# Optimization experiments

Hardware: AMD Instinct MI355X
Metric: run time of the kernel (lower is better)

Reference implementation:

```python
import jax, jax.numpy as jnp
import numpy as np

N_NODES = 50000
N_EDGES = 600000
N_FEAT = 64
D = 128
N_GRAPHS = 1024
N_LAYERS = 4


def setup_inputs() -> dict:
    key = jax.random.key(0)
    ks = jax.random.split(key, 16)
    x = jax.random.normal(ks[0], (N_NODES, N_FEAT), dtype=jnp.float32)
    edge_index = jax.random.randint(ks[1], (2, N_EDGES), 0, N_NODES, dtype=jnp.int64)
    batch_index = jnp.sort(jax.random.randint(ks[2], (N_NODES,), 0, N_GRAPHS, dtype=jnp.int64))
    def lin(k, fan_in, fan_out):
        s = 1.0 / np.sqrt(fan_in)
        kw, kb = jax.random.split(k)
        w = jax.random.uniform(kw, (fan_in, fan_out), minval=-s, maxval=s, dtype=jnp.float32)
        b = jax.random.uniform(kb, (fan_out,), minval=-s, maxval=s, dtype=jnp.float32)
        return w, b
    w0, b0 = lin(ks[3], N_FEAT, D)
    w1, b1 = lin(ks[4], D, D)
    w2, b2 = lin(ks[5], D, D)
    w3, b3 = lin(ks[6], D, D)
    wp, bp = lin(ks[7], D, D)
    return {"x": x, "edge_index": edge_index, "batch_index": batch_index,
            "w0": w0, "b0": b0, "w1": w1, "b1": b1, "w2": w2, "b2": b2,
            "w3": w3, "b3": b3, "wp": wp, "bp": bp}


def _gin_layer(x, src, dst, w, b):
    # GINConv with eps=0: MLP(x_i + sum_{j in N(i)} x_j); MLP = Linear -> ReLU
    agg = jax.ops.segment_sum(x[src], dst, num_segments=N_NODES)
    return jax.nn.relu((x + agg) @ w + b)


def reference(x, edge_index, batch_index, w0, b0, w1, b1, w2, b2, w3, b3, wp, bp):
    src, dst = edge_index[0], edge_index[1]
    # first layer changes width 64 -> 128; agg happens in input width
    agg0 = jax.ops.segment_sum(x[src], dst, num_segments=N_NODES)
    h = jax.nn.relu((x + agg0) @ w0 + b0)
    for w, b in ((w1, b1), (w2, b2), (w3, b3)):
        h = _gin_layer(h, src, dst, w, b)
    # global mean pool per graph
    sums = jax.ops.segment_sum(h, batch_index, num_segments=N_GRAPHS)
    counts = jax.ops.segment_sum(jnp.ones((N_NODES,), dtype=h.dtype), batch_index, num_segments=N_GRAPHS)
    pooled = sums / jnp.maximum(counts, 1.0)[:, None]
    # post_mp: Linear -> ReLU (dropout identity at inference)
    return jax.nn.relu(pooled @ wp + bp)
```

## Files before the change

### kernel.cpp

```cpp
#include <hip/hip_runtime.h>
#include <hip/hip_fp16.h>


#define N_NODES  50000
#define N_EDGES  600000
#define N_FEAT   64
#define DIM      128
#define N_GRAPHS 1024
#define NC       7
#define CSH      13
#define TOT2     (N_NODES * NC)
#define SCH      2048
#define NBLK     ((TOT2 + SCH - 1) / SCH)
#define TPB      256
#define GT128    ((N_NODES + 127) / 128)

typedef _Float16 f16x8 __attribute__((ext_vector_type(8)));
typedef float    f32x4 __attribute__((ext_vector_type(4)));

#define CNTZ2 (TOT2 / 4)
#define XWORK (N_NODES * N_FEAT / 4)
#define PREP_TOTAL (CNTZ2 + XWORK + N_FEAT * DIM + 3 * DIM * DIM)

__global__ __launch_bounds__(TPB) void prep_k(
    const float* __restrict__ x, __half* __restrict__ xh,
    const float* __restrict__ w0, const float* __restrict__ w1,
    const float* __restrict__ w2, const float* __restrict__ w3,
    __half* __restrict__ Wt0, __half* __restrict__ Wt1,
    __half* __restrict__ Wt2, __half* __restrict__ Wt3,
    int* __restrict__ cnt2) {
  int i = blockIdx.x * TPB + threadIdx.x;
  if (i < CNTZ2) {
    *reinterpret_cast<int4*>(cnt2 + i * 4) = make_int4(0, 0, 0, 0);
    return;
  }
  i -= CNTZ2;
  if (i < XWORK) {
    float4 v = *reinterpret_cast<const float4*>(x + (size_t)i * 4);
    union { __half2 h2[2]; uint2 u; } pk;
    pk.h2[0] = __floats2half2_rn(v.x, v.y);
    pk.h2[1] = __floats2half2_rn(v.z, v.w);
    *reinterpret_cast<uint2*>(xh + (size_t)i * 4) = pk.u;
    return;
  }
  int j = i - XWORK;
  if (j < N_FEAT * DIM) {
    int k = j >> 7, n = j & 127;
    Wt0[n * N_FEAT + k] = __float2half(w0[j]);
    return;
  }
  j -= N_FEAT * DIM;
  if (j >= 3 * DIM * DIM) return;
  int wsel = j / (DIM * DIM);
  int jj = j - wsel * (DIM * DIM);
  int k = jj >> 7, n = jj & 127;
  const float* W = (wsel == 0) ? w1 : (wsel == 1) ? w2 : w3;
  __half* Wt     = (wsel == 0) ? Wt1 : (wsel == 1) ? Wt2 : Wt3;
  Wt[n * DIM + k] = __float2half(W[jj]);
}

__global__ __launch_bounds__(TPB) void hist_k(
    const int* __restrict__ src, const int* __restrict__ dst,
    int* __restrict__ cnt2) {
  int e = blockIdx.x * TPB + threadIdx.x;
  if (e >= N_EDGES) return;
  int key = dst[e] * NC + (src[e] >> CSH);
  atomicAdd(&cnt2[key], 1);
}

__global__ __launch_bounds__(TPB) void scan_part_k(
    const int* __restrict__ cnt2, int* __restrict__ part) {
  __shared__ int ws[4];
  int t = threadIdx.x, b = blockIdx.x;
  int base = b * SCH + t * 8;
  int s = 0;
  if (base < TOT2) {
    int4 a = *reinterpret_cast<const int4*>(cnt2 + base);
    int4 c = *reinterpret_cast<const int4*>(cnt2 + base + 4);
    s = a.x + a.y + a.z + a.w + c.x + c.y + c.z + c.w;
  }
  for (int off = 32; off; off >>= 1) s += __shfl_down(s, off, 64);
  int lane = t & 63, wv = t >> 6;
  if (lane == 0) ws[wv] = s;
  __syncthreads();
  if (t == 0) part[b] = ws[0] + ws[1] + ws[2] + ws[3];
}

__global__ __launch_bounds__(TPB) void scan_write_k(
    const int* __restrict__ cnt2, const int* __restrict__ part,
    int* __restrict__ row_ptr2, int* __restrict__ fill2) {
  __shared__ int pscan[TPB];
  __shared__ int wsum[4];
  int t = threadIdx.x, b = blockIdx.x;
  int lane = t & 63, wv = t >> 6;
  int base = b * SCH + t * 8;

  if (base < TOT2) {
    *reinterpret_cast<int4*>(fill2 + base) = make_int4(0, 0, 0, 0);
    *reinterpret_cast<int4*>(fill2 + base + 4) = make_int4(0, 0, 0, 0);
  }

  pscan[t] = (t < NBLK) ? part[t] : 0;
  __syncthreads();
  for (int off = 1; off < TPB; off <<= 1) {
    int v = (t >= off) ? pscan[t - off] : 0;
    __syncthreads();
    pscan[t] += v;
    __syncthreads();
  }
  int blk_off = (b > 0) ? pscan[b - 1] : 0;

  int v[8] = {0,0,0,0,0,0,0,0};
  if (base < TOT2) {
    int4 a = *reinterpret_cast<const int4*>(cnt2 + base);
    int4 c = *reinterpret_cast<const int4*>(cnt2 + base + 4);
    v[0]=a.x; v[1]=a.y; v[2]=a.z; v[3]=a.w;
    v[4]=c.x; v[5]=c.y; v[6]=c.z; v[7]=c.w;
  }
  int ls = 0;
#pragma unroll
  for (int i = 0; i < 8; ++i) ls += v[i];
  int incl = ls;
  for (int off = 1; off < 64; off <<= 1) {
    int u = __shfl_up(incl, off, 64);
    if (lane >= off) incl += u;
  }
  if (lane == 63) wsum[wv] = incl;
  __syncthreads();
  int woff = 0;
  for (int w = 0; w < wv; ++w) woff += wsum[w];
  int run = blk_off + woff + (incl - ls);
  if (base < TOT2) {
    int rp[8];
#pragma unroll
    for (int i = 0; i < 8; ++i) { rp[i] = run; run += v[i]; }
    *reinterpret_cast<int4*>(row_ptr2 + base) = make_int4(rp[0], rp[1], rp[2], rp[3]);
    *reinterpret_cast<int4*>(row_ptr2 + base + 4) = make_int4(rp[4], rp[5], rp[6], rp[7]);
  }
  if (b == 0 && t == 0) row_ptr2[TOT2] = N_EDGES;
}

__global__ __launch_bounds__(TPB) void fill_k(
    const int* __restrict__ src, const int* __restrict__ dst,
    const int* __restrict__ row_ptr2, int* __restrict__ fill2,
    int* __restrict__ csr_src) {
  int e = blockIdx.x * TPB + threadIdx.x;
  if (e >= N_EDGES) return;
  int s = src[e];
  int key = dst[e] * NC + (s >> CSH);
  int pos = row_ptr2[key] + atomicAdd(&fill2[key], 1);
  csr_src[pos] = s;
}

template<int K, bool EPI>
__global__ __launch_bounds__(TPB) void gemm_k(
    const __half* __restrict__ A, const __half* __restrict__ Wt,
    const float* __restrict__ bias, __half* __restrict__ y) {
  constexpr int KP = K + 8;
  constexpr int OSP = 144;
  constexpr int NKC = K / 32;
  constexpr size_t WSZ = (size_t)128 * KP * sizeof(__half);
  constexpr size_t OSZ = (size_t)128 * OSP * sizeof(__half);
  __shared__ __align__(16) char smem[WSZ > OSZ ? WSZ : OSZ];
  __half (*Ws)[KP]  = reinterpret_cast<__half(*)[KP]>(smem);
  __half (*Os)[OSP] = reinterpret_cast<__half(*)[OSP]>(smem);

  int tid = threadIdx.x;
  int w = tid >> 6, lane = tid & 63;
  int quad = lane >> 4, m = lane & 15;
  int row0 = blockIdx.x * 128;

  for (int i = tid; i < 128 * (K / 8); i += TPB) {
    int r = i / (K / 8), c = (i % (K / 8)) * 8;
    *reinterpret_cast<f16x8*>(&Ws[r][c]) =
        *reinterpret_cast<const f16x8*>(Wt + (size_t)r * K + c);
  }

  f16x8 areg[2][NKC];
#pragma unroll
  for (int s = 0; s < 2; ++s) {
    int row = row0 + w * 32 + s * 16 + m;
    row = min(row, N_NODES - 1);
    const f16x8* Ar = reinterpret_cast<const f16x8*>(A + (size_t)row * K);
#pragma unroll
    for (int kc = 0; kc < NKC; ++kc)
      areg[s][kc] = Ar[kc * 4 + quad];
  }
  __syncthreads();

  f32x4 acc[2][8];
#pragma unroll
  for (int s = 0; s < 2; ++s)
#pragma unroll
    for (int t = 0; t < 8; ++t) acc[s][t] = (f32x4){0.f, 0.f, 0.f, 0.f};

#pragma unroll
  for (int kc = 0; kc < NKC; ++kc) {
#pragma unroll
    for (int t = 0; t < 8; ++t) {
      f16x8 b = *reinterpret_cast<const f16x8*>(&Ws[t * 16 + m][kc * 32 + quad * 8]);
      acc[0][t] = __builtin_amdgcn_mfma_f32_16x16x32_f16(areg[0][kc], b, acc[0][t], 0, 0, 0);
      acc[1][t] = __builtin_amdgcn_mfma_f32_16x16x32_f16(areg[1][kc], b, acc[1][t], 0, 0, 0);
    }
  }

  __syncthreads();

#pragma unroll
  for (int t = 0; t < 8; ++t) {
    float bv = EPI ? bias[t * 16 + m] : 0.f;
#pragma unroll
    for (int s = 0; s < 2; ++s)
#pragma unroll
      for (int r = 0; r < 4; ++r) {
        float v = acc[s][t][r];
        if (EPI) v = fmaxf(v + bv, 0.f);
        Os[w * 32 + s * 16 + quad * 4 + r][t * 16 + m] = __float2half(v);
      }
  }
  __syncthreads();

#pragma unroll
  for (int it = 0; it < 8; ++it) {
    int i = tid + it * TPB;
    int r = i >> 4, c = (i & 15) * 8;
    int row = row0 + r;
    if (row < N_NODES)
      *reinterpret_cast<f16x8*>(y + (size_t)row * 128 + c) =
          *reinterpret_cast<const f16x8*>(&Os[r][c]);
  }
}

template<int F, bool BR>
__global__ __launch_bounds__(TPB) void gather_k(
    const __half* __restrict__ y, const int* __restrict__ row_ptr2,
    const int* __restrict__ csr_src, const float* __restrict__ bias,
    __half* __restrict__ hout) {
  constexpr int CH = F / 8;
  const f16x8* yv = reinterpret_cast<const f16x8*>(y);
  int gid  = blockIdx.x * TPB + threadIdx.x;
  int node = gid / CH;
  int l    = gid % CH;
  if (node >= N_NODES) return;
  int beg = row_ptr2[node * NC];
  int end = row_ptr2[node * NC + NC];

  f16x8 self = yv[(size_t)node * CH + l];
  float acc[8];
#pragma unroll
  for (int v = 0; v < 8; ++v) acc[v] = (float)self[v];

  int e = beg;
  for (; e + 3 < end; e += 4) {
    int s0 = csr_src[e+0], s1 = csr_src[e+1], s2 = csr_src[e+2], s3 = csr_src[e+3];
    f16x8 v0 = yv[(size_t)s0 * CH + l];
    f16x8 v1 = yv[(size_t)s1 * CH + l];
    f16x8 v2 = yv[(size_t)s2 * CH + l];
    f16x8 v3 = yv[(size_t)s3 * CH + l];
#pragma unroll
    for (int v = 0; v < 8; ++v)
      acc[v] += ((float)v0[v] + (float)v1[v]) + ((float)v2[v] + (float)v3[v]);
  }
  for (; e < end; ++e) {
    f16x8 v0 = yv[(size_t)csr_src[e] * CH + l];
#pragma unroll
    for (int v = 0; v < 8; ++v) acc[v] += (float)v0[v];
  }

  f16x8 o;
  if (BR) {
    float4 b0 = *reinterpret_cast<const float4*>(bias + l * 8);
    float4 b1 = *reinterpret_cast<const float4*>(bias + l * 8 + 4);
    float bb[8] = {b0.x, b0.y, b0.z, b0.w, b1.x, b1.y, b1.z, b1.w};
#pragma unroll
    for (int v = 0; v < 8; ++v) o[v] = (_Float16)fmaxf(acc[v] + bb[v], 0.f);
  } else {
#pragma unroll
    for (int v = 0; v < 8; ++v) o[v] = (_Float16)acc[v];
  }
  reinterpret_cast<f16x8*>(hout)[(size_t)node * CH + l] = o;
}

__global__ __launch_bounds__(128) void pool_post_k(
    const __half* __restrict__ h, const int* __restrict__ batch,
    const float* __restrict__ W, const float* __restrict__ bias,
    float* __restrict__ out) {
  __shared__ float xs[DIM];
  int g = blockIdx.x;
  int col = threadIdx.x;
  int lo = 0, hi = N_NODES;
  while (lo < hi) { int mid = (lo + hi) >> 1; if (batch[mid] < g) lo = mid + 1; else hi = mid; }
  int beg = lo;
  hi = N_NODES;
  while (lo < hi) { int mid = (lo + hi) >> 1; if (batch[mid] < g + 1) lo = mid + 1; else hi = mid; }
  int end = lo;

  float acc = 0.f;
  for (int n = beg; n < end; ++n) acc += __half2float(h[(size_t)n * DIM + col]);
  float cnt = fmaxf((float)(end - beg), 1.0f);
  xs[col] = acc / cnt;
  __syncthreads();
  float o = bias[col];
  for (int k = 0; k < DIM; ++k)
    o = fmaf(xs[k], W[(size_t)k * DIM + col], o);
  out[(size_t)g * DIM + col] = fmaxf(o, 0.f);
}

extern "C" void kernel_launch(void* const* d_in, const int* in_sizes, int n_in,
                              void* d_out, int out_size, void* d_ws, size_t ws_size,
                              hipStream_t stream) {
  const float* x    = (const float*)d_in[0];
  const int*   ei   = (const int*)d_in[1];
  const int*   batch= (const int*)d_in[2];
  const float* w0 = (const float*)d_in[3];  const float* b0 = (const float*)d_in[4];
  const float* w1 = (const float*)d_in[5];  const float* b1 = (const float*)d_in[6];
  const float* w2 = (const float*)d_in[7];  const float* b2 = (const float*)d_in[8];
  const float* w3 = (const float*)d_in[9];  const float* b3 = (const float*)d_in[10];
  const float* wp = (const float*)d_in[11]; const float* bp = (const float*)d_in[12];
  float* out = (float*)d_out;

  const int* src = ei;
  const int* dst = ei + N_EDGES;

  __half* xh = (__half*)d_ws;
  __half* y  = xh + (size_t)N_NODES * N_FEAT;
  __half* h  = y  + (size_t)N_NODES * DIM;
  __half* Wt0 = h + (size_t)N_NODES * DIM;
  __half* Wt1 = Wt0 + N_FEAT * DIM;
  __half* Wt2 = Wt1 + DIM * DIM;
  __half* Wt3 = Wt2 + DIM * DIM;
  int* cnt2     = (int*)(Wt3 + DIM * DIM);
  int* fill2    = cnt2 + TOT2;
  int* part     = fill2 + TOT2;
  int* row_ptr2 = part + 256;
  int* csr_src  = row_ptr2 + (TOT2 + 1);
  __half* s = y;

  prep_k<<<(PREP_TOTAL + TPB - 1) / TPB, TPB, 0, stream>>>(
      x, xh, w0, w1, w2, w3, Wt0, Wt1, Wt2, Wt3, cnt2);
  hist_k<<<(N_EDGES + TPB - 1) / TPB, TPB, 0, stream>>>(src, dst, cnt2);
  scan_part_k <<<NBLK, TPB, 0, stream>>>(cnt2, part);
  scan_write_k<<<NBLK, TPB, 0, stream>>>(cnt2, part, row_ptr2, fill2);
  fill_k<<<(N_EDGES + TPB - 1) / TPB, TPB, 0, stream>>>(src, dst, row_ptr2,
                                                        fill2, csr_src);

  gather_k<N_FEAT, false><<<(N_NODES * 8 + TPB - 1) / TPB, TPB, 0, stream>>>(
      xh, row_ptr2, csr_src, nullptr, s);
  gemm_k<N_FEAT, true><<<GT128, TPB, 0, stream>>>(s, Wt0, b0, h);

  const __half* Wl[3] = {Wt1, Wt2, Wt3};
  const float*  Bl[3] = {b1, b2, b3};
  for (int l = 0; l < 3; ++l) {
    gemm_k<DIM, false><<<GT128, TPB, 0, stream>>>(h, Wl[l], nullptr, y);
    gather_k<DIM, true><<<(N_NODES * 16 + TPB - 1) / TPB, TPB, 0, stream>>>(
        y, row_ptr2, csr_src, Bl[l], h);
  }

  pool_post_k<<<N_GRAPHS, 128, 0, stream>>>(h, batch, wp, bp, out);
}
```

Before: 302.3 us.

## Fuse all stages into one persistent cooperative kernel with grid syncs

Replaces the sequence of about a dozen separate kernel launches with a single cooperative persistent kernel. Phases are separated by grid-wide barriers and each phase uses grid-stride loops. The scan's second pass now computes block offsets by summing partials directly instead of a shared-memory scan, and pooling handles two graphs per block. This removes launch overhead and inter-kernel gaps. In exchange it adds grid.sync costs, caps occupancy because the fused kernel carries the largest register and shared-memory footprint of any phase, and reloads the GEMM weights for every tile.

Measured after the change: 1.136 ms. 3.76x slower.

```diff
diff --git a/kernel.cpp b/kernel.cpp
--- a/kernel.cpp
+++ b/kernel.cpp
@@ -1,5 +1,8 @@
 #include <hip/hip_runtime.h>
 #include <hip/hip_fp16.h>
+#include <hip/hip_cooperative_groups.h>
+
+namespace cg = cooperative_groups;
 
 
 #define N_NODES  50000
@@ -14,347 +17,365 @@
 #define NBLK     ((TOT2 + SCH - 1) / SCH)
 #define TPB      256
 #define GT128    ((N_NODES + 127) / 128)
+#define NCU      256
 
 typedef _Float16 f16x8 __attribute__((ext_vector_type(8)));
 typedef float    f32x4 __attribute__((ext_vector_type(4)));
 
 #define CNTZ2 (TOT2 / 4)
 #define XWORK (N_NODES * N_FEAT / 4)
-#define PREP_TOTAL (CNTZ2 + XWORK + N_FEAT * DIM + 3 * DIM * DIM)
-
-__global__ __launch_bounds__(TPB) void prep_k(
-    const float* __restrict__ x, __half* __restrict__ xh,
-    const float* __restrict__ w0, const float* __restrict__ w1,
-    const float* __restrict__ w2, const float* __restrict__ w3,
-    __half* __restrict__ Wt0, __half* __restrict__ Wt1,
-    __half* __restrict__ Wt2, __half* __restrict__ Wt3,
-    int* __restrict__ cnt2) {
-  int i = blockIdx.x * TPB + threadIdx.x;
-  if (i < CNTZ2) {
-    *reinterpret_cast<int4*>(cnt2 + i * 4) = make_int4(0, 0, 0, 0);
-    return;
-  }
-  i -= CNTZ2;
-  if (i < XWORK) {
-    float4 v = *reinterpret_cast<const float4*>(x + (size_t)i * 4);
-    union { __half2 h2[2]; uint2 u; } pk;
-    pk.h2[0] = __floats2half2_rn(v.x, v.y);
-    pk.h2[1] = __floats2half2_rn(v.z, v.w);
-    *reinterpret_cast<uint2*>(xh + (size_t)i * 4) = pk.u;
-    return;
-  }
-  int j = i - XWORK;
-  if (j < N_FEAT * DIM) {
-    int k = j >> 7, n = j & 127;
-    Wt0[n * N_FEAT + k] = __float2half(w0[j]);
-    return;
-  }
-  j -= N_FEAT * DIM;
-  if (j >= 3 * DIM * DIM) return;
-  int wsel = j / (DIM * DIM);
-  int jj = j - wsel * (DIM * DIM);
-  int k = jj >> 7, n = jj & 127;
-  const float* W = (wsel == 0) ? w1 : (wsel == 1) ? w2 : w3;
-  __half* Wt     = (wsel == 0) ? Wt1 : (wsel == 1) ? Wt2 : Wt3;
-  Wt[n * DIM + k] = __float2half(W[jj]);
-}
-
-__global__ __launch_bounds__(TPB) void hist_k(
-    const int* __restrict__ src, const int* __restrict__ dst,
-    int* __restrict__ cnt2) {
-  int e = blockIdx.x * TPB + threadIdx.x;
-  if (e >= N_EDGES) return;
-  int key = dst[e] * NC + (src[e] >> CSH);
-  atomicAdd(&cnt2[key], 1);
-}
-
-__global__ __launch_bounds__(TPB) void scan_part_k(
-    const int* __restrict__ cnt2, int* __restrict__ part) {
-  __shared__ int ws[4];
-  int t = threadIdx.x, b = blockIdx.x;
-  int base = b * SCH + t * 8;
-  int s = 0;
-  if (base < TOT2) {
-    int4 a = *reinterpret_cast<const int4*>(cnt2 + base);
-    int4 c = *reinterpret_cast<const int4*>(cnt2 + base + 4);
-    s = a.x + a.y + a.z + a.w + c.x + c.y + c.z + c.w;
-  }
-  for (int off = 32; off; off >>= 1) s += __shfl_down(s, off, 64);
-  int lane = t & 63, wv = t >> 6;
-  if (lane == 0) ws[wv] = s;
-  __syncthreads();
-  if (t == 0) part[b] = ws[0] + ws[1] + ws[2] + ws[3];
-}
-
-__global__ __launch_bounds__(TPB) void scan_write_k(
-    const int* __restrict__ cnt2, const int* __restrict__ part,
-    int* __restrict__ row_ptr2, int* __restrict__ fill2) {
-  __shared__ int pscan[TPB];
-  __shared__ int wsum[4];
-  int t = threadIdx.x, b = blockIdx.x;
-  int lane = t & 63, wv = t >> 6;
-  int base = b * SCH + t * 8;
-
-  if (base < TOT2) {
-    *reinterpret_cast<int4*>(fill2 + base) = make_int4(0, 0, 0, 0);
-    *reinterpret_cast<int4*>(fill2 + base + 4) = make_int4(0, 0, 0, 0);
-  }
-
-  pscan[t] = (t < NBLK) ? part[t] : 0;
-  __syncthreads();
-  for (int off = 1; off < TPB; off <<= 1) {
-    int v = (t >= off) ? pscan[t - off] : 0;
-    __syncthreads();
-    pscan[t] += v;
-    __syncthreads();
-  }
-  int blk_off = (b > 0) ? pscan[b - 1] : 0;
-
-  int v[8] = {0,0,0,0,0,0,0,0};
-  if (base < TOT2) {
-    int4 a = *reinterpret_cast<const int4*>(cnt2 + base);
-    int4 c = *reinterpret_cast<const int4*>(cnt2 + base + 4);
-    v[0]=a.x; v[1]=a.y; v[2]=a.z; v[3]=a.w;
-    v[4]=c.x; v[5]=c.y; v[6]=c.z; v[7]=c.w;
-  }
-  int ls = 0;
-#pragma unroll
-  for (int i = 0; i < 8; ++i) ls += v[i];
-  int incl = ls;
-  for (int off = 1; off < 64; off <<= 1) {
-    int u = __shfl_up(incl, off, 64);
-    if (lane >= off) incl += u;
-  }
-  if (lane == 63) wsum[wv] = incl;
-  __syncthreads();
-  int woff = 0;
-  for (int w = 0; w < wv; ++w) woff += wsum[w];
-  int run = blk_off + woff + (incl - ls);
-  if (base < TOT2) {
-    int rp[8];
-#pragma unroll
-    for (int i = 0; i < 8; ++i) { rp[i] = run; run += v[i]; }
-    *reinterpret_cast<int4*>(row_ptr2 + base) = make_int4(rp[0], rp[1], rp[2], rp[3]);
-    *reinterpret_cast<int4*>(row_ptr2 + base + 4) = make_int4(rp[4], rp[5], rp[6], rp[7]);
-  }
-  if (b == 0 && t == 0) row_ptr2[TOT2] = N_EDGES;
-}
-
-__global__ __launch_bounds__(TPB) void fill_k(
-    const int* __restrict__ src, const int* __restrict__ dst,
-    const int* __restrict__ row_ptr2, int* __restrict__ fill2,
-    int* __restrict__ csr_src) {
-  int e = blockIdx.x * TPB + threadIdx.x;
-  if (e >= N_EDGES) return;
-  int s = src[e];
-  int key = dst[e] * NC + (s >> CSH);
-  int pos = row_ptr2[key] + atomicAdd(&fill2[key], 1);
-  csr_src[pos] = s;
+#define PREP_TOTAL (2 * CNTZ2 + XWORK + N_FEAT * DIM + 3 * DIM * DIM)
+
+#define SMEM_BYTES 36864
+
+struct MegaArgs {
+  const float* x; const int* src; const int* dst; const int* batch;
+  const float *w0, *b0, *w1, *b1, *w2, *b2, *w3, *b3, *wp, *bp;
+  float* out;
+  __half *xh, *y, *h, *Wt0, *Wt1, *Wt2, *Wt3;
+  int *cnt2, *fill2, *part, *row_ptr2, *csr_src;
+};
+
+__device__ void scan_part_phase(const int* __restrict__ cnt2,
+                                int* __restrict__ part, char* smem) {
+  int* ws = reinterpret_cast<int*>(smem);
+  int t = threadIdx.x, lane = t & 63, wv = t >> 6;
+  for (int pb = blockIdx.x; pb < NBLK; pb += gridDim.x) {
+    int base = pb * SCH + t * 8;
+    int s = 0;
+    if (base < TOT2) {
+      int4 aa = *reinterpret_cast<const int4*>(cnt2 + base);
+      int4 cc = *reinterpret_cast<const int4*>(cnt2 + base + 4);
+      s = aa.x + aa.y + aa.z + aa.w + cc.x + cc.y + cc.z + cc.w;
+    }
+    for (int off = 32; off; off >>= 1) s += __shfl_down(s, off, 64);
+    if (lane == 0) ws[wv] = s;
+    __syncthreads();
+    if (t == 0) part[pb] = ws[0] + ws[1] + ws[2] + ws[3];
+    __syncthreads();
+  }
+}
+
+__device__ void scan_write_phase(const int* __restrict__ cnt2,
+                                 const int* __restrict__ part,
+                                 int* __restrict__ row_ptr2, char* smem) {
+  int* sh = reinterpret_cast<int*>(smem);
+  int t = threadIdx.x, lane = t & 63, wv = t >> 6;
+  for (int pb = blockIdx.x; pb < NBLK; pb += gridDim.x) {
+    int v = (t < pb) ? part[t] : 0;
+    for (int off = 32; off; off >>= 1) v += __shfl_down(v, off, 64);
+    if (lane == 0) sh[wv] = v;
+    __syncthreads();
+    int blk_off = sh[0] + sh[1] + sh[2] + sh[3];
+    __syncthreads();
+
+    int base = pb * SCH + t * 8;
+    int vals[8] = {0,0,0,0,0,0,0,0};
+    if (base < TOT2) {
+      int4 aa = *reinterpret_cast<const int4*>(cnt2 + base);
+      int4 cc = *reinterpret_cast<const int4*>(cnt2 + base + 4);
+      vals[0]=aa.x; vals[1]=aa.y; vals[2]=aa.z; vals[3]=aa.w;
+      vals[4]=cc.x; vals[5]=cc.y; vals[6]=cc.z; vals[7]=cc.w;
+    }
+    int ls = 0;
+#pragma unroll
+    for (int i2 = 0; i2 < 8; ++i2) ls += vals[i2];
+    int incl = ls;
+    for (int off = 1; off < 64; off <<= 1) {
+      int u = __shfl_up(incl, off, 64);
+      if (lane >= off) incl += u;
+    }
+    if (lane == 63) sh[4 + wv] = incl;
+    __syncthreads();
+    int woff = 0;
+    for (int w2 = 0; w2 < wv; ++w2) woff += sh[4 + w2];
+    int run = blk_off + woff + (incl - ls);
+    if (base < TOT2) {
+      int rp[8];
+#pragma unroll
+      for (int i2 = 0; i2 < 8; ++i2) { rp[i2] = run; run += vals[i2]; }
+      *reinterpret_cast<int4*>(row_ptr2 + base) = make_int4(rp[0],rp[1],rp[2],rp[3]);
+      *reinterpret_cast<int4*>(row_ptr2 + base + 4) = make_int4(rp[4],rp[5],rp[6],rp[7]);
+    }
+    __syncthreads();
+  }
+  if (blockIdx.x == 0 && threadIdx.x == 0) row_ptr2[TOT2] = N_EDGES;
 }
 
 template<int K, bool EPI>
-__global__ __launch_bounds__(TPB) void gemm_k(
-    const __half* __restrict__ A, const __half* __restrict__ Wt,
-    const float* __restrict__ bias, __half* __restrict__ y) {
+__device__ void gemm_phase(const __half* __restrict__ A,
+                           const __half* __restrict__ Wt,
+                           const float* __restrict__ bias,
+                           __half* __restrict__ yOut, char* smem) {
   constexpr int KP = K + 8;
   constexpr int OSP = 144;
   constexpr int NKC = K / 32;
-  constexpr size_t WSZ = (size_t)128 * KP * sizeof(__half);
-  constexpr size_t OSZ = (size_t)128 * OSP * sizeof(__half);
-  __shared__ __align__(16) char smem[WSZ > OSZ ? WSZ : OSZ];
   __half (*Ws)[KP]  = reinterpret_cast<__half(*)[KP]>(smem);
   __half (*Os)[OSP] = reinterpret_cast<__half(*)[OSP]>(smem);
-
   int tid = threadIdx.x;
   int w = tid >> 6, lane = tid & 63;
   int quad = lane >> 4, m = lane & 15;
-  int row0 = blockIdx.x * 128;
-
-  for (int i = tid; i < 128 * (K / 8); i += TPB) {
-    int r = i / (K / 8), c = (i % (K / 8)) * 8;
-    *reinterpret_cast<f16x8*>(&Ws[r][c]) =
-        *reinterpret_cast<const f16x8*>(Wt + (size_t)r * K + c);
-  }
-
-  f16x8 areg[2][NKC];
-#pragma unroll
-  for (int s = 0; s < 2; ++s) {
-    int row = row0 + w * 32 + s * 16 + m;
-    row = min(row, N_NODES - 1);
-    const f16x8* Ar = reinterpret_cast<const f16x8*>(A + (size_t)row * K);
-#pragma unroll
-    for (int kc = 0; kc < NKC; ++kc)
-      areg[s][kc] = Ar[kc * 4 + quad];
-  }
-  __syncthreads();
-
-  f32x4 acc[2][8];
-#pragma unroll
-  for (int s = 0; s < 2; ++s)
-#pragma unroll
-    for (int t = 0; t < 8; ++t) acc[s][t] = (f32x4){0.f, 0.f, 0.f, 0.f};
-
-#pragma unroll
-  for (int kc = 0; kc < NKC; ++kc) {
+  for (int tile = blockIdx.x; tile < GT128; tile += gridDim.x) {
+    int row0 = tile * 128;
+    for (int i = tid; i < 128 * (K / 8); i += TPB) {
+      int r = i / (K / 8), c = (i % (K / 8)) * 8;
+      *reinterpret_cast<f16x8*>(&Ws[r][c]) =
+          *reinterpret_cast<const f16x8*>(Wt + (size_t)r * K + c);
+    }
+    f16x8 areg[2][NKC];
+#pragma unroll
+    for (int s = 0; s < 2; ++s) {
+      int row = row0 + w * 32 + s * 16 + m;
+      row = min(row, N_NODES - 1);
+      const f16x8* Ar = reinterpret_cast<const f16x8*>(A + (size_t)row * K);
+#pragma unroll
+      for (int kc = 0; kc < NKC; ++kc) areg[s][kc] = Ar[kc * 4 + quad];
+    }
+    __syncthreads();
+
+    f32x4 acc[2][8];
+#pragma unroll
+    for (int s = 0; s < 2; ++s)
+#pragma unroll
+      for (int t = 0; t < 8; ++t) acc[s][t] = (f32x4){0.f, 0.f, 0.f, 0.f};
+
+#pragma unroll
+    for (int kc = 0; kc < NKC; ++kc) {
+#pragma unroll
+      for (int t = 0; t < 8; ++t) {
+        f16x8 b = *reinterpret_cast<const f16x8*>(&Ws[t * 16 + m][kc * 32 + quad * 8]);
+        acc[0][t] = __builtin_amdgcn_mfma_f32_16x16x32_f16(areg[0][kc], b, acc[0][t], 0, 0, 0);
+        acc[1][t] = __builtin_amdgcn_mfma_f32_16x16x32_f16(areg[1][kc], b, acc[1][t], 0, 0, 0);
+      }
+    }
+    __syncthreads();
+
 #pragma unroll
     for (int t = 0; t < 8; ++t) {
-      f16x8 b = *reinterpret_cast<const f16x8*>(&Ws[t * 16 + m][kc * 32 + quad * 8]);
-      acc[0][t] = __builtin_amdgcn_mfma_f32_16x16x32_f16(areg[0][kc], b, acc[0][t], 0, 0, 0);
-      acc[1][t] = __builtin_amdgcn_mfma_f32_16x16x32_f16(areg[1][kc], b, acc[1][t], 0, 0, 0);
-    }
-  }
-
-  __syncthreads();
-
-#pragma unroll
-  for (int t = 0; t < 8; ++t) {
-    float bv = EPI ? bias[t * 16 + m] : 0.f;
-#pragma unroll
-    for (int s = 0; s < 2; ++s)
-#pragma unroll
-      for (int r = 0; r < 4; ++r) {
-        float v = acc[s][t][r];
-        if (EPI) v = fmaxf(v + bv, 0.f);
-        Os[w * 32 + s * 16 + quad * 4 + r][t * 16 + m] = __float2half(v);
-      }
-  }
-  __syncthreads();
-
-#pragma unroll
-  for (int it = 0; it < 8; ++it) {
-    int i = tid + it * TPB;
-    int r = i >> 4, c = (i & 15) * 8;
-    int row = row0 + r;
-    if (row < N_NODES)
-      *reinterpret_cast<f16x8*>(y + (size_t)row * 128 + c) =
-          *reinterpret_cast<const f16x8*>(&Os[r][c]);
+      float bv = EPI ? bias[t * 16 + m] : 0.f;
+#pragma unroll
+      for (int s = 0; s < 2; ++s)
+#pragma unroll
+        for (int r = 0; r < 4; ++r) {
+          float v = acc[s][t][r];
+          if (EPI) v = fmaxf(v + bv, 0.f);
+          Os[w * 32 + s * 16 + quad * 4 + r][t * 16 + m] = __float2half(v);
+        }
+    }
+    __syncthreads();
+
+#pragma unroll
+    for (int it = 0; it < 8; ++it) {
+      int i = tid + it * TPB;
+      int r = i >> 4, c = (i & 15) * 8;
+      int row = row0 + r;
+      if (row < N_NODES)
+        *reinterpret_cast<f16x8*>(yOut + (size_t)row * 128 + c) =
+            *reinterpret_cast<const f16x8*>(&Os[r][c]);
+    }
+    __syncthreads();
   }
 }
 
 template<int F, bool BR>
-__global__ __launch_bounds__(TPB) void gather_k(
-    const __half* __restrict__ y, const int* __restrict__ row_ptr2,
-    const int* __restrict__ csr_src, const float* __restrict__ bias,
-    __half* __restrict__ hout) {
+__device__ void gather_phase(const __half* __restrict__ yin,
+                             const int* __restrict__ row_ptr2,
+                             const int* __restrict__ csr_src,
+                             const float* __restrict__ bias,
+                             __half* __restrict__ hout) {
   constexpr int CH = F / 8;
-  const f16x8* yv = reinterpret_cast<const f16x8*>(y);
-  int gid  = blockIdx.x * TPB + threadIdx.x;
-  int node = gid / CH;
-  int l    = gid % CH;
-  if (node >= N_NODES) return;
-  int beg = row_ptr2[node * NC];
-  int end = row_ptr2[node * NC + NC];
-
-  f16x8 self = yv[(size_t)node * CH + l];
-  float acc[8];
-#pragma unroll
-  for (int v = 0; v < 8; ++v) acc[v] = (float)self[v];
-
-  int e = beg;
-  for (; e + 3 < end; e += 4) {
-    int s0 = csr_src[e+0], s1 = csr_src[e+1], s2 = csr_src[e+2], s3 = csr_src[e+3];
-    f16x8 v0 = yv[(size_t)s0 * CH + l];
-    f16x8 v1 = yv[(size_t)s1 * CH + l];
-    f16x8 v2 = yv[(size_t)s2 * CH + l];
-    f16x8 v3 = yv[(size_t)s3 * CH + l];
-#pragma unroll
-    for (int v = 0; v < 8; ++v)
-      acc[v] += ((float)v0[v] + (float)v1[v]) + ((float)v2[v] + (float)v3[v]);
-  }
-  for (; e < end; ++e) {
-    f16x8 v0 = yv[(size_t)csr_src[e] * CH + l];
-#pragma unroll
-    for (int v = 0; v < 8; ++v) acc[v] += (float)v0[v];
-  }
-
-  f16x8 o;
-  if (BR) {
-    float4 b0 = *reinterpret_cast<const float4*>(bias + l * 8);
-    float4 b1 = *reinterpret_cast<const float4*>(bias + l * 8 + 4);
-    float bb[8] = {b0.x, b0.y, b0.z, b0.w, b1.x, b1.y, b1.z, b1.w};
-#pragma unroll
-    for (int v = 0; v < 8; ++v) o[v] = (_Float16)fmaxf(acc[v] + bb[v], 0.f);
-  } else {
-#pragma unroll
-    for (int v = 0; v < 8; ++v) o[v] = (_Float16)acc[v];
-  }
-  reinterpret_cast<f16x8*>(hout)[(size_t)node * CH + l] = o;
-}
-
-__global__ __launch_bounds__(128) void pool_post_k(
-    const __half* __restrict__ h, const int* __restrict__ batch,
-    const float* __restrict__ W, const float* __restrict__ bias,
-    float* __restrict__ out) {
-  __shared__ float xs[DIM];
-  int g = blockIdx.x;
-  int col = threadIdx.x;
-  int lo = 0, hi = N_NODES;
-  while (lo < hi) { int mid = (lo + hi) >> 1; if (batch[mid] < g) lo = mid + 1; else hi = mid; }
-  int beg = lo;
-  hi = N_NODES;
-  while (lo < hi) { int mid = (lo + hi) >> 1; if (batch[mid] < g + 1) lo = mid + 1; else hi = mid; }
-  int end = lo;
-
-  float acc = 0.f;
-  for (int n = beg; n < end; ++n) acc += __half2float(h[(size_t)n * DIM + col]);
-  float cnt = fmaxf((float)(end - beg), 1.0f);
-  xs[col] = acc / cnt;
-  __syncthreads();
-  float o = bias[col];
-  for (int k = 0; k < DIM; ++k)
-    o = fmaf(xs[k], W[(size_t)k * DIM + col], o);
-  out[(size_t)g * DIM + col] = fmaxf(o, 0.f);
+  const f16x8* yv = reinterpret_cast<const f16x8*>(yin);
+  const int total = N_NODES * CH;
+  for (int gid = blockIdx.x * TPB + threadIdx.x; gid < total;
+       gid += gridDim.x * TPB) {
+    int node = gid / CH;
+    int l    = gid % CH;
+    int beg = row_ptr2[node * NC];
+    int end = row_ptr2[node * NC + NC];
+
+    f16x8 self = yv[(size_t)node * CH + l];
+    float acc[8];
+#pragma unroll
+    for (int v = 0; v < 8; ++v) acc[v] = (float)self[v];
+
+    int e = beg;
+    for (; e + 3 < end; e += 4) {
+      int s0 = csr_src[e+0], s1 = csr_src[e+1], s2 = csr_src[e+2], s3 = csr_src[e+3];
+      f16x8 v0 = yv[(size_t)s0 * CH + l];
+      f16x8 v1 = yv[(size_t)s1 * CH + l];
+      f16x8 v2 = yv[(size_t)s2 * CH + l];
+      f16x8 v3 = yv[(size_t)s3 * CH + l];
+#pragma unroll
+      for (int v = 0; v < 8; ++v)
+        acc[v] += ((float)v0[v] + (float)v1[v]) + ((float)v2[v] + (float)v3[v]);
+    }
+    for (; e < end; ++e) {
+      f16x8 v0 = yv[(size_t)csr_src[e] * CH + l];
+#pragma unroll
+      for (int v = 0; v < 8; ++v) acc[v] += (float)v0[v];
+    }
+
+    f16x8 o;
+    if (BR) {
+      float4 b0 = *reinterpret_cast<const float4*>(bias + l * 8);
+      float4 b1 = *reinterpret_cast<const float4*>(bias + l * 8 + 4);
+      float bb[8] = {b0.x, b0.y, b0.z, b0.w, b1.x, b1.y, b1.z, b1.w};
+#pragma unroll
+      for (int v = 0; v < 8; ++v) o[v] = (_Float16)fmaxf(acc[v] + bb[v], 0.f);
+    } else {
+#pragma unroll
+      for (int v = 0; v < 8; ++v) o[v] = (_Float16)acc[v];
+    }
+    reinterpret_cast<f16x8*>(hout)[(size_t)node * CH + l] = o;
+  }
+}
+
+__device__ void pool_phase(const __half* __restrict__ h, const int* __restrict__ batch,
+                           const float* __restrict__ W, const float* __restrict__ bias,
+                           float* __restrict__ out, char* smem) {
+  float* xs = reinterpret_cast<float*>(smem);
+  int t = threadIdx.x;
+  int sub = t >> 7, col = t & 127;
+  for (int gp = blockIdx.x; gp < N_GRAPHS / 2; gp += gridDim.x) {
+    int g = gp * 2 + sub;
+    int lo = 0, hi = N_NODES;
+    while (lo < hi) { int mid = (lo + hi) >> 1; if (batch[mid] < g) lo = mid + 1; else hi = mid; }
+    int beg = lo;
+    hi = N_NODES;
+    while (lo < hi) { int mid = (lo + hi) >> 1; if (batch[mid] < g + 1) lo = mid + 1; else hi = mid; }
+    int end = lo;
+    float acc = 0.f;
+    for (int n = beg; n < end; ++n) acc += __half2float(h[(size_t)n * DIM + col]);
+    float cnt = fmaxf((float)(end - beg), 1.0f);
+    xs[sub * DIM + col] = acc / cnt;
+    __syncthreads();
+    float o = bias[col];
+    for (int k = 0; k < DIM; ++k)
+      o = fmaf(xs[sub * DIM + k], W[(size_t)k * DIM + col], o);
+    out[(size_t)g * DIM + col] = fmaxf(o, 0.f);
+    __syncthreads();
+  }
+}
+
+__global__ __launch_bounds__(TPB, 4) void mega_k(MegaArgs a) {
+  __shared__ __align__(16) char smem[SMEM_BYTES];
+  cg::grid_group grid = cg::this_grid();
+  const int gstride = gridDim.x * TPB;
+  const int gtid = blockIdx.x * TPB + threadIdx.x;
+
+  for (int i = gtid; i < PREP_TOTAL; i += gstride) {
+    int j = i;
+    if (j < CNTZ2) {
+      *reinterpret_cast<int4*>(a.cnt2 + j * 4) = make_int4(0, 0, 0, 0);
+      continue;
+    }
+    j -= CNTZ2;
+    if (j < CNTZ2) {
+      *reinterpret_cast<int4*>(a.fill2 + j * 4) = make_int4(0, 0, 0, 0);
+      continue;
+    }
+    j -= CNTZ2;
+    if (j < XWORK) {
+      float4 v = *reinterpret_cast<const float4*>(a.x + (size_t)j * 4);
+      union { __half2 h2[2]; uint2 u; } pk;
+      pk.h2[0] = __floats2half2_rn(v.x, v.y);
+      pk.h2[1] = __floats2half2_rn(v.z, v.w);
+      *reinterpret_cast<uint2*>(a.xh + (size_t)j * 4) = pk.u;
+      continue;
+    }
+    j -= XWORK;
+    if (j < N_FEAT * DIM) {
+      int k = j >> 7, n = j & 127;
+      a.Wt0[n * N_FEAT + k] = __float2half(a.w0[j]);
+      continue;
+    }
+    j -= N_FEAT * DIM;
+    int wsel = j / (DIM * DIM);
+    int jj = j - wsel * (DIM * DIM);
+    int k = jj >> 7, n = jj & 127;
+    const float* W = (wsel == 0) ? a.w1 : (wsel == 1) ? a.w2 : a.w3;
+    __half* Wt     = (wsel == 0) ? a.Wt1 : (wsel == 1) ? a.Wt2 : a.Wt3;
+    Wt[n * DIM + k] = __float2half(W[jj]);
+  }
+  grid.sync();
+
+  for (int e = gtid; e < N_EDGES; e += gstride)
+    atomicAdd(&a.cnt2[a.dst[e] * NC + (a.src[e] >> CSH)], 1);
+  grid.sync();
+
+  scan_part_phase(a.cnt2, a.part, smem);
+  grid.sync();
+  scan_write_phase(a.cnt2, a.part, a.row_ptr2, smem);
+  grid.sync();
+
+  for (int e = gtid; e < N_EDGES; e += gstride) {
+    int s = a.src[e];
+    int key = a.dst[e] * NC + (s >> CSH);
+    int pos = a.row_ptr2[key] + atomicAdd(&a.fill2[key], 1);
+    a.csr_src[pos] = s;
+  }
+  grid.sync();
+
+  gather_phase<N_FEAT, false>(a.xh, a.row_ptr2, a.csr_src, nullptr, a.y);
+  grid.sync();
+  gemm_phase<N_FEAT, true>(a.y, a.Wt0, a.b0, a.h, smem);
+  grid.sync();
+
+#pragma unroll 1
+  for (int l = 0; l < 3; ++l) {
+    const __half* Wt = (l == 0) ? a.Wt1 : (l == 1) ? a.Wt2 : a.Wt3;
+    const float*  bb = (l == 0) ? a.b1  : (l == 1) ? a.b2  : a.b3;
+    gemm_phase<DIM, false>(a.h, Wt, nullptr, a.y, smem);
+    grid.sync();
+    gather_phase<DIM, true>(a.y, a.row_ptr2, a.csr_src, bb, a.h);
+    grid.sync();
+  }
+
+  pool_phase(a.h, a.batch, a.wp, a.bp, a.out, smem);
 }
 
 extern "C" void kernel_launch(void* const* d_in, const int* in_sizes, int n_in,
                               void* d_out, int out_size, void* d_ws, size_t ws_size,
                               hipStream_t stream) {
-  const float* x    = (const float*)d_in[0];
-  const int*   ei   = (const int*)d_in[1];
-  const int*   batch= (const int*)d_in[2];
-  const float* w0 = (const float*)d_in[3];  const float* b0 = (const float*)d_in[4];
-  const float* w1 = (const float*)d_in[5];  const float* b1 = (const float*)d_in[6];
-  const float* w2 = (const float*)d_in[7];  const float* b2 = (const float*)d_in[8];
-  const float* w3 = (const float*)d_in[9];  const float* b3 = (const float*)d_in[10];
-  const float* wp = (const float*)d_in[11]; const float* bp = (const float*)d_in[12];
-  float* out = (float*)d_out;
-
-  const int* src = ei;
-  const int* dst = ei + N_EDGES;
-
-  __half* xh = (__half*)d_ws;
-  __half* y  = xh + (size_t)N_NODES * N_FEAT;
-  __half* h  = y  + (size_t)N_NODES * DIM;
-  __half* Wt0 = h + (size_t)N_NODES * DIM;
-  __half* Wt1 = Wt0 + N_FEAT * DIM;
-  __half* Wt2 = Wt1 + DIM * DIM;
-  __half* Wt3 = Wt2 + DIM * DIM;
-  int* cnt2     = (int*)(Wt3 + DIM * DIM);
-  int* fill2    = cnt2 + TOT2;
-  int* part     = fill2 + TOT2;
-  int* row_ptr2 = part + 256;
-  int* csr_src  = row_ptr2 + (TOT2 + 1);
-  __half* s = y;
-
-  prep_k<<<(PREP_TOTAL + TPB - 1) / TPB, TPB, 0, stream>>>(
-      x, xh, w0, w1, w2, w3, Wt0, Wt1, Wt2, Wt3, cnt2);
-  hist_k<<<(N_EDGES + TPB - 1) / TPB, TPB, 0, stream>>>(src, dst, cnt2);
-  scan_part_k <<<NBLK, TPB, 0, stream>>>(cnt2, part);
-  scan_write_k<<<NBLK, TPB, 0, stream>>>(cnt2, part, row_ptr2, fill2);
-  fill_k<<<(N_EDGES + TPB - 1) / TPB, TPB, 0, stream>>>(src, dst, row_ptr2,
-                                                        fill2, csr_src);
-
-  gather_k<N_FEAT, false><<<(N_NODES * 8 + TPB - 1) / TPB, TPB, 0, stream>>>(
-      xh, row_ptr2, csr_src, nullptr, s);
-  gemm_k<N_FEAT, true><<<GT128, TPB, 0, stream>>>(s, Wt0, b0, h);
-
-  const __half* Wl[3] = {Wt1, Wt2, Wt3};
-  const float*  Bl[3] = {b1, b2, b3};
-  for (int l = 0; l < 3; ++l) {
-    gemm_k<DIM, false><<<GT128, TPB, 0, stream>>>(h, Wl[l], nullptr, y);
-    gather_k<DIM, true><<<(N_NODES * 16 + TPB - 1) / TPB, TPB, 0, stream>>>(
-        y, row_ptr2, csr_src, Bl[l], h);
-  }
-
-  pool_post_k<<<N_GRAPHS, 128, 0, stream>>>(h, batch, wp, bp, out);
-}
+  MegaArgs a;
+  a.x = (const float*)d_in[0];
+  const int* ei = (const int*)d_in[1];
+  a.src = ei; a.dst = ei + N_EDGES;
+  a.batch = (const int*)d_in[2];
+  a.w0 = (const float*)d_in[3];  a.b0 = (const float*)d_in[4];
+  a.w1 = (const float*)d_in[5];  a.b1 = (const float*)d_in[6];
+  a.w2 = (const float*)d_in[7];  a.b2 = (const float*)d_in[8];
+  a.w3 = (const float*)d_in[9];  a.b3 = (const float*)d_in[10];
+  a.wp = (const float*)d_in[11]; a.bp = (const float*)d_in[12];
+  a.out = (float*)d_out;
+
+  __half* p = (__half*)d_ws;
+  a.xh  = p; p += (size_t)N_NODES * N_FEAT;
+  a.y   = p; p += (size_t)N_NODES * DIM;
+  a.h   = p; p += (size_t)N_NODES * DIM;
+  a.Wt0 = p; p += N_FEAT * DIM;
+  a.Wt1 = p; p += DIM * DIM;
+  a.Wt2 = p; p += DIM * DIM;
+  a.Wt3 = p; p += DIM * DIM;
+  int* q = (int*)p;
+  a.cnt2     = q; q += TOT2;
+  a.fill2    = q; q += TOT2;
+  a.part     = q; q += 256;
+  a.row_ptr2 = q; q += TOT2 + 1;
+  a.csr_src  = q;
+
+  static int s_grid = 0;
+  if (s_grid == 0) {
+    int bpc = 0;
+    if (hipOccupancyMaxActiveBlocksPerMultiprocessor(
+            &bpc, (const void*)mega_k, TPB, 0) != hipSuccess || bpc < 1)
+      bpc = 1;
+    long g = (long)bpc * NCU;
+    if (g > 2048) g = 2048;
+    s_grid = (int)g;
+  }
+
+  void* params[] = { (void*)&a };
+  hipLaunchCooperativeKernel((const void*)mega_k, dim3(s_grid), dim3(TPB),
+                             params, 0, stream);
+}
```

## Drop fill array by atomically bumping row pointers; add compact node row_ptr

Applied to the files above, without the earlier changes.

The CSR build no longer keeps a separate fill-counter array. fill_k now atomically increments row_ptr2 itself to get each edge's slot, which removes zeroing one array and one extra read per edge. scan_write_k also writes a compact per-node row_ptr, so the gather kernels read pointers at stride 1 instead of stride NC. The gather loop gains an 8-way unrolled path to keep more neighbor loads in flight, at the cost of more registers.

After: 305.4 us. About the same (+1.0%).

```diff
diff --git a/kernel.cpp b/kernel.cpp
--- a/kernel.cpp
+++ b/kernel.cpp
@@ -88,17 +88,12 @@
 
 __global__ __launch_bounds__(TPB) void scan_write_k(
     const int* __restrict__ cnt2, const int* __restrict__ part,
-    int* __restrict__ row_ptr2, int* __restrict__ fill2) {
+    int* __restrict__ row_ptr2, int* __restrict__ row_ptr) {
   __shared__ int pscan[TPB];
   __shared__ int wsum[4];
   int t = threadIdx.x, b = blockIdx.x;
   int lane = t & 63, wv = t >> 6;
   int base = b * SCH + t * 8;
-
-  if (base < TOT2) {
-    *reinterpret_cast<int4*>(fill2 + base) = make_int4(0, 0, 0, 0);
-    *reinterpret_cast<int4*>(fill2 + base + 4) = make_int4(0, 0, 0, 0);
-  }
 
   pscan[t] = (t < NBLK) ? part[t] : 0;
   __syncthreads();
@@ -136,19 +131,23 @@
     for (int i = 0; i < 8; ++i) { rp[i] = run; run += v[i]; }
     *reinterpret_cast<int4*>(row_ptr2 + base) = make_int4(rp[0], rp[1], rp[2], rp[3]);
     *reinterpret_cast<int4*>(row_ptr2 + base + 4) = make_int4(rp[4], rp[5], rp[6], rp[7]);
-  }
-  if (b == 0 && t == 0) row_ptr2[TOT2] = N_EDGES;
+#pragma unroll
+    for (int i = 0; i < 8; ++i) {
+      int bin = base + i;
+      if (bin % NC == 0) row_ptr[bin / NC] = rp[i];
+    }
+  }
+  if (b == 0 && t == 0) row_ptr[N_NODES] = N_EDGES;
 }
 
 __global__ __launch_bounds__(TPB) void fill_k(
     const int* __restrict__ src, const int* __restrict__ dst,
-    const int* __restrict__ row_ptr2, int* __restrict__ fill2,
-    int* __restrict__ csr_src) {
+    int* __restrict__ row_ptr2, int* __restrict__ csr_src) {
   int e = blockIdx.x * TPB + threadIdx.x;
   if (e >= N_EDGES) return;
   int s = src[e];
   int key = dst[e] * NC + (s >> CSH);
-  int pos = row_ptr2[key] + atomicAdd(&fill2[key], 1);
+  int pos = atomicAdd(&row_ptr2[key], 1);
   csr_src[pos] = s;
 }
 
@@ -233,7 +232,7 @@
 
 template<int F, bool BR>
 __global__ __launch_bounds__(TPB) void gather_k(
-    const __half* __restrict__ y, const int* __restrict__ row_ptr2,
+    const __half* __restrict__ y, const int* __restrict__ row_ptr,
     const int* __restrict__ csr_src, const float* __restrict__ bias,
     __half* __restrict__ hout) {
   constexpr int CH = F / 8;
@@ -242,8 +241,8 @@
   int node = gid / CH;
   int l    = gid % CH;
   if (node >= N_NODES) return;
-  int beg = row_ptr2[node * NC];
-  int end = row_ptr2[node * NC + NC];
+  int beg = row_ptr[node];
+  int end = row_ptr[node + 1];
 
   f16x8 self = yv[(size_t)node * CH + l];
   float acc[8];
@@ -251,6 +250,22 @@
   for (int v = 0; v < 8; ++v) acc[v] = (float)self[v];
 
   int e = beg;
+  for (; e + 7 < end; e += 8) {
+    int s0 = csr_src[e+0], s1 = csr_src[e+1], s2 = csr_src[e+2], s3 = csr_src[e+3];
+    int s4 = csr_src[e+4], s5 = csr_src[e+5], s6 = csr_src[e+6], s7 = csr_src[e+7];
+    f16x8 v0 = yv[(size_t)s0 * CH + l];
+    f16x8 v1 = yv[(size_t)s1 * CH + l];
+    f16x8 v2 = yv[(size_t)s2 * CH + l];
+    f16x8 v3 = yv[(size_t)s3 * CH + l];
+    f16x8 v4 = yv[(size_t)s4 * CH + l];
+    f16x8 v5 = yv[(size_t)s5 * CH + l];
+    f16x8 v6 = yv[(size_t)s6 * CH + l];
+    f16x8 v7 = yv[(size_t)s7 * CH + l];
+#pragma unroll
+    for (int v = 0; v < 8; ++v)
+      acc[v] += (((float)v0[v] + (float)v1[v]) + ((float)v2[v] + (float)v3[v])) +
+                (((float)v4[v] + (float)v5[v]) + ((float)v6[v] + (float)v7[v]));
+  }
   for (; e + 3 < end; e += 4) {
     int s0 = csr_src[e+0], s1 = csr_src[e+1], s2 = csr_src[e+2], s3 = csr_src[e+3];
     f16x8 v0 = yv[(size_t)s0 * CH + l];
@@ -330,22 +345,22 @@
   __half* Wt2 = Wt1 + DIM * DIM;
   __half* Wt3 = Wt2 + DIM * DIM;
   int* cnt2     = (int*)(Wt3 + DIM * DIM);
-  int* fill2    = cnt2 + TOT2;
-  int* part     = fill2 + TOT2;
+  int* part     = cnt2 + TOT2;
   int* row_ptr2 = part + 256;
-  int* csr_src  = row_ptr2 + (TOT2 + 1);
+  int* row_ptr  = row_ptr2 + TOT2;
+  int* csr_src  = row_ptr + (N_NODES + 1);
   __half* s = y;
 
   prep_k<<<(PREP_TOTAL + TPB - 1) / TPB, TPB, 0, stream>>>(
       x, xh, w0, w1, w2, w3, Wt0, Wt1, Wt2, Wt3, cnt2);
   hist_k<<<(N_EDGES + TPB - 1) / TPB, TPB, 0, stream>>>(src, dst, cnt2);
   scan_part_k <<<NBLK, TPB, 0, stream>>>(cnt2, part);
-  scan_write_k<<<NBLK, TPB, 0, stream>>>(cnt2, part, row_ptr2, fill2);
+  scan_write_k<<<NBLK, TPB, 0, stream>>>(cnt2, part, row_ptr2, row_ptr);
   fill_k<<<(N_EDGES + TPB - 1) / TPB, TPB, 0, stream>>>(src, dst, row_ptr2,
-                                                        fill2, csr_src);
+                                                        csr_src);
 
   gather_k<N_FEAT, false><<<(N_NODES * 8 + TPB - 1) / TPB, TPB, 0, stream>>>(
-      xh, row_ptr2, csr_src, nullptr, s);
+      xh, row_ptr, csr_src, nullptr, s);
   gemm_k<N_FEAT, true><<<GT128, TPB, 0, stream>>>(s, Wt0, b0, h);
 
   const __half* Wl[3] = {Wt1, Wt2, Wt3};
@@ -353,7 +368,7 @@
   for (int l = 0; l < 3; ++l) {
     gemm_k<DIM, false><<<GT128, TPB, 0, stream>>>(h, Wl[l], nullptr, y);
     gather_k<DIM, true><<<(N_NODES * 16 + TPB - 1) / TPB, TPB, 0, stream>>>(
-        y, row_ptr2, csr_src, Bl[l], h);
+        y, row_ptr, csr_src, Bl[l], h);
   }
 
   pool_post_k<<<N_GRAPHS, 128, 0, stream>>>(h, batch, wp, bp, out);
```
